# Kernel tuning notes

Hardware: AMD Instinct MI355X
Metric: run time of the kernel (lower is better)

The kernel has to match this reference:

```python
import jax, jax.numpy as jnp
import numpy as np

N_NODES = 100000
N_EDGES = 3200000
IN_DIM = 20
HIDDEN = 64
BN_EPS = 1e-5


def _glorot(key, shape):
    fan_in, fan_out = shape[0], shape[1]
    lim = float(np.sqrt(6.0 / (fan_in + fan_out)))
    return jax.random.uniform(key, shape, jnp.float32, -lim, lim)


def setup_inputs() -> dict:
    key = jax.random.key(0)
    ks = jax.random.split(key, 16)
    xs = jax.random.normal(ks[0], (N_NODES, 6), jnp.float32)
    xt = jax.random.normal(ks[1], (N_NODES, 14), jnp.float32)
    edge_index = jax.random.randint(ks[2], (2, N_EDGES), 0, N_NODES, jnp.int64)
    return {
        "xs": xs,
        "xt": xt,
        "edge_index": edge_index,
        # SAGEConv1: lin_l (neighbors, with bias) + lin_r (root, no bias)
        "W1l": _glorot(ks[3], (IN_DIM, HIDDEN)),
        "b1l": jnp.zeros((HIDDEN,), jnp.float32),
        "W1r": _glorot(ks[4], (IN_DIM, HIDDEN)),
        "g1": jnp.ones((HIDDEN,), jnp.float32),
        "be1": jnp.zeros((HIDDEN,), jnp.float32),
        # SAGEConv2: hidden -> hidden//2
        "W2l": _glorot(ks[5], (HIDDEN, HIDDEN // 2)),
        "b2l": jnp.zeros((HIDDEN // 2,), jnp.float32),
        "W2r": _glorot(ks[6], (HIDDEN, HIDDEN // 2)),
        "g2": jnp.ones((HIDDEN // 2,), jnp.float32),
        "be2": jnp.zeros((HIDDEN // 2,), jnp.float32),
        # embed_proj: Linear(1, 32) + ReLU
        "Wp": _glorot(ks[7], (1, 32)),
        "bp": jnp.zeros((32,), jnp.float32),
        # outage_head: Linear(32, 1)
        "Wo": _glorot(ks[8], (32, 1)),
        "bo": jnp.zeros((1,), jnp.float32),
    }


def _sage_conv(x, src, dst, Wl, bl, Wr):
    # PyG SAGEConv (aggr='mean'): out = lin_l(mean_{j in N(i)} x_j) + lin_r(x_i)
    n = x.shape[0]
    agg = jax.ops.segment_sum(x[src], dst, num_segments=n)           # [N, F] gather+scatter
    deg = jax.ops.segment_sum(jnp.ones_like(dst, x.dtype), dst, num_segments=n)
    mean = agg / jnp.maximum(deg, 1.0)[:, None]
    return mean @ Wl + bl + x @ Wr


def _batchnorm(h, gamma, beta):
    # training-mode BN: biased batch stats over nodes
    m = h.mean(0)
    v = jnp.var(h, axis=0)
    return (h - m) * jax.lax.rsqrt(v + BN_EPS) * gamma + beta


def reference(xs, xt, edge_index, W1l, b1l, W1r, g1, be1,
              W2l, b2l, W2r, g2, be2, Wp, bp, Wo, bo):
    src, dst = edge_index[0], edge_index[1]
    x = jnp.concatenate([xs, xt], axis=-1)                  # [N, 20]
    h = jax.nn.relu(_batchnorm(_sage_conv(x, src, dst, W1l, b1l, W1r), g1, be1))
    h = jax.nn.relu(_batchnorm(_sage_conv(h, src, dst, W2l, b2l, W2r), g2, be2))
    # heads (dropout is identity in eval)
    logit_raw = h.mean(-1, keepdims=True)                   # [N, 1]
    embed = jax.nn.relu(logit_raw @ Wp + bp)                # [N, 32]
    outage_logit = (embed @ Wo + bo)[:, 0]                  # [N]
    return outage_logit
```

## Files before the change

kernel.cpp:

```cpp
#include <hip/hip_runtime.h>
#include <hip/hip_bf16.h>

#define BN_EPS 1e-5f
#define BK_SHIFT 5
#define BK_NODES 32
#define CAP 1280

typedef unsigned short ushort_t;

__device__ inline ushort_t f2bf(float x) {
  unsigned u = __float_as_uint(x);
  unsigned r = (u + 0x7FFFu + ((u >> 16) & 1u)) >> 16;
  return (ushort_t)r;
}
__device__ inline void bf2x(unsigned u, float& a, float& b) {
  a = __uint_as_float(u << 16);
  b = __uint_as_float(u & 0xFFFF0000u);
}

__device__ inline void unpack20(float* ag, uint4 A, uint4 B, uint4 C) {
  float u, v;
  bf2x(A.x, u, v); atomicAdd(ag + 0, u);  atomicAdd(ag + 1, v);
  bf2x(A.y, u, v); atomicAdd(ag + 2, u);  atomicAdd(ag + 3, v);
  bf2x(A.z, u, v); atomicAdd(ag + 4, u);  atomicAdd(ag + 5, v);
  bf2x(A.w, u, v); atomicAdd(ag + 6, u);  atomicAdd(ag + 7, v);
  bf2x(B.x, u, v); atomicAdd(ag + 8, u);  atomicAdd(ag + 9, v);
  bf2x(B.y, u, v); atomicAdd(ag + 10, u); atomicAdd(ag + 11, v);
  bf2x(B.z, u, v); atomicAdd(ag + 12, u); atomicAdd(ag + 13, v);
  bf2x(B.w, u, v); atomicAdd(ag + 14, u); atomicAdd(ag + 15, v);
  bf2x(C.x, u, v); atomicAdd(ag + 16, u); atomicAdd(ag + 17, v);
  bf2x(C.y, u, v); atomicAdd(ag + 18, u); atomicAdd(ag + 19, v);
}

__device__ inline void unpack32(float* ag, uint4 A, uint4 B, uint4 C, uint4 D) {
  float u, v;
  bf2x(A.x, u, v); atomicAdd(ag + 0, u);  atomicAdd(ag + 1, v);
  bf2x(A.y, u, v); atomicAdd(ag + 2, u);  atomicAdd(ag + 3, v);
  bf2x(A.z, u, v); atomicAdd(ag + 4, u);  atomicAdd(ag + 5, v);
  bf2x(A.w, u, v); atomicAdd(ag + 6, u);  atomicAdd(ag + 7, v);
  bf2x(B.x, u, v); atomicAdd(ag + 8, u);  atomicAdd(ag + 9, v);
  bf2x(B.y, u, v); atomicAdd(ag + 10, u); atomicAdd(ag + 11, v);
  bf2x(B.z, u, v); atomicAdd(ag + 12, u); atomicAdd(ag + 13, v);
  bf2x(B.w, u, v); atomicAdd(ag + 14, u); atomicAdd(ag + 15, v);
  bf2x(C.x, u, v); atomicAdd(ag + 16, u); atomicAdd(ag + 17, v);
  bf2x(C.y, u, v); atomicAdd(ag + 18, u); atomicAdd(ag + 19, v);
  bf2x(C.z, u, v); atomicAdd(ag + 20, u); atomicAdd(ag + 21, v);
  bf2x(C.w, u, v); atomicAdd(ag + 22, u); atomicAdd(ag + 23, v);
  bf2x(D.x, u, v); atomicAdd(ag + 24, u); atomicAdd(ag + 25, v);
  bf2x(D.y, u, v); atomicAdd(ag + 26, u); atomicAdd(ag + 27, v);
  bf2x(D.z, u, v); atomicAdd(ag + 28, u); atomicAdd(ag + 29, v);
  bf2x(D.w, u, v); atomicAdd(ag + 30, u); atomicAdd(ag + 31, v);
}

__global__ __launch_bounds__(256) void k_xcat(
    const float* __restrict__ xs, const float* __restrict__ xt,
    ushort_t* __restrict__ xcatp, int N) {
  long i = (long)blockIdx.x * 256 + threadIdx.x;
  if (i >= (long)N * 24) return;
  int n = (int)(i / 24), f = (int)(i - (long)n * 24);
  float v = 0.f;
  if (f < 6) v = xs[(long)n * 6 + f];
  else if (f < 20) v = xt[(long)n * 14 + f - 6];
  xcatp[i] = f2bf(v);
}

__global__ __launch_bounds__(256) void k_scatter_b(
    const int* __restrict__ srcA, const int* __restrict__ dstA,
    unsigned* __restrict__ cursor, unsigned* __restrict__ bucketBuf, int E) {
  long e0 = ((long)blockIdx.x * 256 + threadIdx.x) * 4;
  if (e0 >= E) return;
  if (e0 + 4 <= E) {
    int4 s4 = *(const int4*)(srcA + e0);
    int4 d4 = *(const int4*)(dstA + e0);
    unsigned p0 = atomicAdd(&cursor[(d4.x >> BK_SHIFT) * 16], 1u);
    unsigned p1 = atomicAdd(&cursor[(d4.y >> BK_SHIFT) * 16], 1u);
    unsigned p2 = atomicAdd(&cursor[(d4.z >> BK_SHIFT) * 16], 1u);
    unsigned p3 = atomicAdd(&cursor[(d4.w >> BK_SHIFT) * 16], 1u);
    if (p0 < CAP) bucketBuf[(size_t)(d4.x >> BK_SHIFT) * CAP + p0] =
        ((unsigned)(d4.x & (BK_NODES - 1)) << 17) | (unsigned)s4.x;
    if (p1 < CAP) bucketBuf[(size_t)(d4.y >> BK_SHIFT) * CAP + p1] =
        ((unsigned)(d4.y & (BK_NODES - 1)) << 17) | (unsigned)s4.y;
    if (p2 < CAP) bucketBuf[(size_t)(d4.z >> BK_SHIFT) * CAP + p2] =
        ((unsigned)(d4.z & (BK_NODES - 1)) << 17) | (unsigned)s4.z;
    if (p3 < CAP) bucketBuf[(size_t)(d4.w >> BK_SHIFT) * CAP + p3] =
        ((unsigned)(d4.w & (BK_NODES - 1)) << 17) | (unsigned)s4.w;
  } else {
    for (long e = e0; e < E; ++e) {
      int s = srcA[e], d = dstA[e];
      unsigned pos = atomicAdd(&cursor[(d >> BK_SHIFT) * 16], 1u);
      if (pos < CAP) bucketBuf[(size_t)(d >> BK_SHIFT) * CAP + pos] =
          ((unsigned)(d & (BK_NODES - 1)) << 17) | (unsigned)s;
    }
  }
}

__global__ __launch_bounds__(256, 4) void k_g1(
    const unsigned* __restrict__ cursor, const unsigned* __restrict__ bucketBuf,
    const ushort_t* __restrict__ xcatp,
    const float* __restrict__ xs, const float* __restrict__ xt,
    const float* __restrict__ W1l, const float* __restrict__ b1l,
    const float* __restrict__ W1r,
    float* __restrict__ h1, float* __restrict__ deg_g,
    float* __restrict__ sum1, float* __restrict__ sq1, int N) {
  __shared__ float sWl[1280], sWr[1280];
  __shared__ float aggL[BK_NODES * 21];
  __shared__ float sx[BK_NODES * 20];
  __shared__ float rdeg[BK_NODES];
  __shared__ unsigned degL[BK_NODES];
  __shared__ float ls[256], lq[256];
  int tid = threadIdx.x;
  int b = blockIdx.x;
  int base = b << BK_SHIFT;

  for (int i = tid; i < BK_NODES * 21; i += 256) aggL[i] = 0.f;
  if (tid < BK_NODES) degL[tid] = 0u;
  for (int i = tid; i < 1280; i += 256) { sWl[i] = W1l[i]; sWr[i] = W1r[i]; }
  for (int i = tid; i < BK_NODES * 20; i += 256) {
    int nl = i / 20, f = i - nl * 20;
    int n = base + nl;
    float v = 0.f;
    if (n < N) v = (f < 6) ? xs[(long)n * 6 + f] : xt[(long)n * 14 + f - 6];
    sx[i] = v;
  }
  __syncthreads();

  unsigned cnt = cursor[b * 16];
  if (cnt > CAP) cnt = CAP;
  const unsigned* bb = bucketBuf + (size_t)b * CAP;

  for (unsigned ib = 0; ib < cnt; ib += 1024) {
    unsigned i = ib + ((unsigned)tid << 2);
    if (i >= cnt) continue;
    if (i + 4 <= cnt) {
      uint4 pk4 = *(const uint4*)(bb + i);
      unsigned s0 = pk4.x & 0x1FFFFu, d0 = pk4.x >> 17;
      unsigned s1 = pk4.y & 0x1FFFFu, d1 = pk4.y >> 17;
      unsigned s2 = pk4.z & 0x1FFFFu, d2 = pk4.z >> 17;
      unsigned s3 = pk4.w & 0x1FFFFu, d3 = pk4.w >> 17;
      const uint4* x0 = (const uint4*)(xcatp + (size_t)s0 * 24);
      const uint4* x1 = (const uint4*)(xcatp + (size_t)s1 * 24);
      const uint4* x2 = (const uint4*)(xcatp + (size_t)s2 * 24);
      const uint4* x3 = (const uint4*)(xcatp + (size_t)s3 * 24);
      uint4 a00 = x0[0], a01 = x0[1], a02 = x0[2];
      uint4 a10 = x1[0], a11 = x1[1], a12 = x1[2];
      uint4 a20 = x2[0], a21 = x2[1], a22 = x2[2];
      uint4 a30 = x3[0], a31 = x3[1], a32 = x3[2];
      atomicAdd(&degL[d0], 1u); atomicAdd(&degL[d1], 1u);
      atomicAdd(&degL[d2], 1u); atomicAdd(&degL[d3], 1u);
      unpack20(&aggL[d0 * 21], a00, a01, a02);
      unpack20(&aggL[d1 * 21], a10, a11, a12);
      unpack20(&aggL[d2 * 21], a20, a21, a22);
      unpack20(&aggL[d3 * 21], a30, a31, a32);
    } else {
      for (unsigned j = i; j < cnt; ++j) {
        unsigned pk = bb[j];
        unsigned s = pk & 0x1FFFFu, dl = pk >> 17;
        const uint4* xr = (const uint4*)(xcatp + (size_t)s * 24);
        uint4 A = xr[0], B = xr[1], C = xr[2];
        atomicAdd(&degL[dl], 1u);
        unpack20(&aggL[dl * 21], A, B, C);
      }
    }
  }
  __syncthreads();

  if (tid < BK_NODES) {
    unsigned d = degL[tid];
    rdeg[tid] = 1.f / fmaxf((float)d, 1.f);
    int n = base + tid;
    if (n < N) deg_g[n] = (float)d;
  }
  __syncthreads();
  for (int i = tid; i < BK_NODES * 20; i += 256) {
    int nl = i / 20, f = i - nl * 20;
    aggL[nl * 21 + f] *= rdeg[nl];
  }
  __syncthreads();

  int c = tid & 63;
  float s_acc = 0.f, q_acc = 0.f;
  for (int p = 0; p < 8; ++p) {
    int nl = (tid >> 6) + p * 4;
    int n = base + nl;
    if (n < N) {
      float acc = b1l[c];
#pragma unroll
      for (int f = 0; f < 20; ++f)
        acc += aggL[nl * 21 + f] * sWl[f * 64 + c] + sx[nl * 20 + f] * sWr[f * 64 + c];
      h1[(long)n * 64 + c] = acc;
      s_acc += acc; q_acc += acc * acc;
    }
  }
  ls[tid] = s_acc; lq[tid] = q_acc;
  __syncthreads();
  if (tid < 64) {
    float s = ls[tid], q = lq[tid];
#pragma unroll
    for (int r = 1; r < 4; ++r) { s += ls[tid + 64 * r]; q += lq[tid + 64 * r]; }
    atomicAdd(&sum1[tid], s);
    atomicAdd(&sq1[tid], q);
  }
}

__global__ __launch_bounds__(256) void k_bn1_proj(
    float* __restrict__ h1,
    const float* __restrict__ sum, const float* __restrict__ sq,
    const float* __restrict__ g, const float* __restrict__ be,
    const float* __restrict__ W2l, const float* __restrict__ W2r,
    ushort_t* __restrict__ p2l, int N) {
  __shared__ float sWl[64 * 32], sWr[64 * 32];
  __shared__ float sh[8][64];
  __shared__ float sscale[64], sshift[64];
  int tid = threadIdx.x;
  for (int i = tid; i < 2048; i += 256) { sWl[i] = W2l[i]; sWr[i] = W2r[i]; }
  if (tid < 64) {
    float m = sum[tid] / (float)N;
    float v = sq[tid] / (float)N - m * m;
    float inv = rsqrtf(v + BN_EPS);
    float sc = g[tid] * inv;
    sscale[tid] = sc;
    sshift[tid] = be[tid] - m * sc;
  }
  __syncthreads();
  long base = (long)blockIdx.x * 512;
#pragma unroll
  for (int k = 0; k < 2; ++k) {
    long j = base + tid + k * 256;
    if (j < (long)N * 64) {
      int c = (int)(j & 63);
      float v = h1[j] * sscale[c] + sshift[c];
      sh[(tid + k * 256) >> 6][c] = fmaxf(v, 0.f);
    }
  }
  __syncthreads();
  int c2 = tid & 31, ln = tid >> 5;
  int n = blockIdx.x * 8 + ln;
  if (n < N) {
    float al = 0.f, ar = 0.f;
#pragma unroll
    for (int c = 0; c < 64; ++c) {
      float hv = sh[ln][c];
      al += hv * sWl[c * 32 + c2];
      ar += hv * sWr[c * 32 + c2];
    }
    p2l[(long)n * 32 + c2] = f2bf(al);
    h1[(long)n * 64 + c2] = ar;
  }
}

__global__ __launch_bounds__(256, 4) void k_g2(
    const unsigned* __restrict__ cursor, const unsigned* __restrict__ bucketBuf,
    const ushort_t* __restrict__ p2l, const float* __restrict__ b2l,
    const float* __restrict__ deg_g,
    float* __restrict__ h1,
    float* __restrict__ sum2, float* __restrict__ sq2, int N) {
  __shared__ float aggL[BK_NODES * 33];
  __shared__ float ls[256], lq[256];
  int tid = threadIdx.x;
  int b = blockIdx.x;
  int base = b << BK_SHIFT;
  for (int i = tid; i < BK_NODES * 33; i += 256) aggL[i] = 0.f;
  __syncthreads();
  unsigned cnt = cursor[b * 16];
  if (cnt > CAP) cnt = CAP;
  const unsigned* bb = bucketBuf + (size_t)b * CAP;

  for (unsigned ib = 0; ib < cnt; ib += 1024) {
    unsigned i = ib + ((unsigned)tid << 2);
    if (i >= cnt) continue;
    if (i + 4 <= cnt) {
      uint4 pk4 = *(const uint4*)(bb + i);
      unsigned s0 = pk4.x & 0x1FFFFu, d0 = pk4.x >> 17;
      unsigned s1 = pk4.y & 0x1FFFFu, d1 = pk4.y >> 17;
      unsigned s2 = pk4.z & 0x1FFFFu, d2 = pk4.z >> 17;
      unsigned s3 = pk4.w & 0x1FFFFu, d3 = pk4.w >> 17;
      const uint4* r0 = (const uint4*)(p2l + (size_t)s0 * 32);
      const uint4* r1 = (const uint4*)(p2l + (size_t)s1 * 32);
      const uint4* r2 = (const uint4*)(p2l + (size_t)s2 * 32);
      const uint4* r3 = (const uint4*)(p2l + (size_t)s3 * 32);
      uint4 a00 = r0[0], a01 = r0[1], a02 = r0[2], a03 = r0[3];
      uint4 a10 = r1[0], a11 = r1[1], a12 = r1[2], a13 = r1[3];
      uint4 a20 = r2[0], a21 = r2[1], a22 = r2[2], a23 = r2[3];
      uint4 a30 = r3[0], a31 = r3[1], a32 = r3[2], a33 = r3[3];
      unpack32(&aggL[d0 * 33], a00, a01, a02, a03);
      unpack32(&aggL[d1 * 33], a10, a11, a12, a13);
      unpack32(&aggL[d2 * 33], a20, a21, a22, a23);
      unpack32(&aggL[d3 * 33], a30, a31, a32, a33);
    } else {
      for (unsigned j = i; j < cnt; ++j) {
        unsigned pk = bb[j];
        unsigned s = pk & 0x1FFFFu, dl = pk >> 17;
        const uint4* pr = (const uint4*)(p2l + (size_t)s * 32);
        uint4 A = pr[0], B = pr[1], C = pr[2], D = pr[3];
        unpack32(&aggL[dl * 33], A, B, C, D);
      }
    }
  }
  __syncthreads();

  int c = tid & 31;
  float bc = b2l[c];
  float s_acc = 0.f, q_acc = 0.f;
  for (int p = 0; p < 4; ++p) {
    int nl = (tid >> 5) + p * 8;
    int n = base + nl;
    if (n < N) {
      float rd = 1.f / fmaxf(deg_g[n], 1.f);
      long idx = (long)n * 64 + c;
      float h2 = aggL[nl * 33 + c] * rd + bc + h1[idx];
      h1[idx] = h2;
      s_acc += h2; q_acc += h2 * h2;
    }
  }
  ls[tid] = s_acc; lq[tid] = q_acc;
  __syncthreads();
  if (tid < 32) {
    float s = ls[tid], q = lq[tid];
#pragma unroll
    for (int r = 1; r < 8; ++r) { s += ls[tid + 32 * r]; q += lq[tid + 32 * r]; }
    atomicAdd(&sum2[tid], s);
    atomicAdd(&sq2[tid], q);
  }
}

__global__ __launch_bounds__(256) void k_final(
    const float* __restrict__ h2,
    const float* __restrict__ sum, const float* __restrict__ sq,
    const float* __restrict__ g, const float* __restrict__ be,
    const float* __restrict__ Wp, const float* __restrict__ bp,
    const float* __restrict__ Wo, const float* __restrict__ bo,
    float* __restrict__ out, int N) {
  int tid = threadIdx.x;
  int c = tid & 31, ln = tid >> 5;
  int n = blockIdx.x * 8 + ln;
  if (n >= N) return;
  float m = sum[c] / (float)N;
  float v = sq[c] / (float)N - m * m;
  float inv = rsqrtf(v + BN_EPS);
  float sc = g[c] * inv;
  float sh = be[c] - m * sc;
  float x = fmaxf(h2[(long)n * 64 + c] * sc + sh, 0.f);
#pragma unroll
  for (int msk = 16; msk >= 1; msk >>= 1) x += __shfl_xor(x, msk);
  float lr = x * (1.0f / 32.0f);
  float e = fmaxf(lr * Wp[c] + bp[c], 0.f) * Wo[c];
#pragma unroll
  for (int msk = 16; msk >= 1; msk >>= 1) e += __shfl_xor(e, msk);
  if (c == 0) out[n] = e + bo[0];
}

__global__ __launch_bounds__(256) void k_edge_agg20(
    const int* __restrict__ srcA, const int* __restrict__ dstA,
    const float* __restrict__ xs, const float* __restrict__ xt,
    float* __restrict__ agg, float* __restrict__ deg, int E) {
  long gtid = (long)blockIdx.x * blockDim.x + threadIdx.x;
  int f = (int)(gtid & 31);
  long e = gtid >> 5;
  if (e >= E) return;
  int s = srcA[e], d = dstA[e];
  if (f < 20) {
    float v = (f < 6) ? xs[(long)s * 6 + f] : xt[(long)s * 14 + (f - 6)];
    atomicAdd(&agg[(long)d * 20 + f], v);
  }
  if (f == 0) atomicAdd(&deg[d], 1.0f);
}

__global__ __launch_bounds__(256) void k_sage1(
    const float* __restrict__ agg, const float* __restrict__ deg,
    const float* __restrict__ xs, const float* __restrict__ xt,
    const float* __restrict__ W1l, const float* __restrict__ b1l,
    const float* __restrict__ W1r, float* __restrict__ h1, int N) {
  __shared__ float sWl[1280], sWr[1280];
  __shared__ float sm[4][20], sx[4][20];
  int tid = threadIdx.x;
  for (int i = tid; i < 1280; i += 256) { sWl[i] = W1l[i]; sWr[i] = W1r[i]; }
  int ln = tid >> 6, c = tid & 63;
  int n = blockIdx.x * 4 + ln;
  if (n < N && c < 20) {
    float dv = fmaxf(deg[n], 1.0f);
    sm[ln][c] = agg[(long)n * 20 + c] / dv;
    sx[ln][c] = (c < 6) ? xs[(long)n * 6 + c] : xt[(long)n * 14 + (c - 6)];
  }
  __syncthreads();
  if (n < N) {
    float acc = b1l[c];
#pragma unroll
    for (int f = 0; f < 20; ++f)
      acc += sm[ln][f] * sWl[f * 64 + c] + sx[ln][f] * sWr[f * 64 + c];
    h1[(long)n * 64 + c] = acc;
  }
}

__global__ __launch_bounds__(256) void k_stats(
    const float* __restrict__ h, int N, int C,
    float* __restrict__ sum, float* __restrict__ sq) {
  int tid = threadIdx.x;
  int rows = 256 / C;
  int c = tid % C, r = tid / C;
  float s = 0.f, q = 0.f;
  for (long n = (long)blockIdx.x * rows + r; n < N; n += (long)gridDim.x * rows) {
    float v = h[n * C + c];
    s += v; q += v * v;
  }
  __shared__ float ls[256], lq[256];
  ls[tid] = s; lq[tid] = q;
  __syncthreads();
  if (r == 0) {
    for (int rr = 1; rr < rows; ++rr) { s += ls[c + rr * C]; q += lq[c + rr * C]; }
    atomicAdd(&sum[c], s);
    atomicAdd(&sq[c], q);
  }
}

__global__ __launch_bounds__(256) void k_bn1_proj_fb(
    const float* __restrict__ h1,
    const float* __restrict__ sum, const float* __restrict__ sq,
    const float* __restrict__ g, const float* __restrict__ be,
    const float* __restrict__ W2l, const float* __restrict__ W2r,
    float* __restrict__ p2l, float* __restrict__ p2r, int N) {
  __shared__ float sWl[64 * 32], sWr[64 * 32];
  __shared__ float sh[8][64];
  __shared__ float sscale[64], sshift[64];
  int tid = threadIdx.x;
  for (int i = tid; i < 2048; i += 256) { sWl[i] = W2l[i]; sWr[i] = W2r[i]; }
  if (tid < 64) {
    float m = sum[tid] / (float)N;
    float v = sq[tid] / (float)N - m * m;
    float inv = rsqrtf(v + BN_EPS);
    float sc = g[tid] * inv;
    sscale[tid] = sc;
    sshift[tid] = be[tid] - m * sc;
  }
  __syncthreads();
  long base = (long)blockIdx.x * 512;
#pragma unroll
  for (int k = 0; k < 2; ++k) {
    long j = base + tid + k * 256;
    if (j < (long)N * 64) {
      int c = (int)(j & 63);
      float v = h1[j] * sscale[c] + sshift[c];
      sh[(tid + k * 256) >> 6][c] = fmaxf(v, 0.f);
    }
  }
  __syncthreads();
  int c2 = tid & 31, ln = tid >> 5;
  int n = blockIdx.x * 8 + ln;
  if (n < N) {
    float al = 0.f, ar = 0.f;
#pragma unroll
    for (int c = 0; c < 64; ++c) {
      float hv = sh[ln][c];
      al += hv * sWl[c * 32 + c2];
      ar += hv * sWr[c * 32 + c2];
    }
    p2l[(long)n * 32 + c2] = al;
    p2r[(long)n * 32 + c2] = ar;
  }
}

__global__ __launch_bounds__(256) void k_edge_agg32(
    const int* __restrict__ srcA, const int* __restrict__ dstA,
    const float* __restrict__ p, float* __restrict__ agg, int E) {
  long gtid = (long)blockIdx.x * blockDim.x + threadIdx.x;
  int f = (int)(gtid & 31);
  long e = gtid >> 5;
  if (e >= E) return;
  atomicAdd(&agg[(long)dstA[e] * 32 + f], p[(long)srcA[e] * 32 + f]);
}

__global__ __launch_bounds__(256) void k_h2(
    const float* __restrict__ agg, const float* __restrict__ deg,
    const float* __restrict__ b2l, const float* __restrict__ p2r,
    float* __restrict__ h2, int N) {
  long i = (long)blockIdx.x * blockDim.x + threadIdx.x;
  if (i >= (long)N * 32) return;
  int n = (int)(i >> 5), f = (int)(i & 31);
  float dv = fmaxf(deg[n], 1.0f);
  h2[i] = agg[i] / dv + b2l[f] + p2r[i];
}

__global__ __launch_bounds__(256) void k_final_fb(
    const float* __restrict__ h2,
    const float* __restrict__ sum, const float* __restrict__ sq,
    const float* __restrict__ g, const float* __restrict__ be,
    const float* __restrict__ Wp, const float* __restrict__ bp,
    const float* __restrict__ Wo, const float* __restrict__ bo,
    float* __restrict__ out, int N) {
  int tid = threadIdx.x;
  int c = tid & 31, ln = tid >> 5;
  int n = blockIdx.x * 8 + ln;
  if (n >= N) return;
  float m = sum[c] / (float)N;
  float v = sq[c] / (float)N - m * m;
  float inv = rsqrtf(v + BN_EPS);
  float sc = g[c] * inv;
  float sh = be[c] - m * sc;
  float x = fmaxf(h2[(long)n * 32 + c] * sc + sh, 0.f);
#pragma unroll
  for (int msk = 16; msk >= 1; msk >>= 1) x += __shfl_xor(x, msk);
  float lr = x * (1.0f / 32.0f);
  float e = fmaxf(lr * Wp[c] + bp[c], 0.f) * Wo[c];
#pragma unroll
  for (int msk = 16; msk >= 1; msk >>= 1) e += __shfl_xor(e, msk);
  if (c == 0) out[n] = e + bo[0];
}

extern "C" void kernel_launch(void* const* d_in, const int* in_sizes, int n_in,
                              void* d_out, int out_size, void* d_ws, size_t ws_size,
                              hipStream_t stream) {
  const float* xs  = (const float*)d_in[0];
  const float* xt  = (const float*)d_in[1];
  const int*   ei  = (const int*)d_in[2];
  const float* W1l = (const float*)d_in[3];
  const float* b1l = (const float*)d_in[4];
  const float* W1r = (const float*)d_in[5];
  const float* g1  = (const float*)d_in[6];
  const float* be1 = (const float*)d_in[7];
  const float* W2l = (const float*)d_in[8];
  const float* b2l = (const float*)d_in[9];
  const float* W2r = (const float*)d_in[10];
  const float* g2  = (const float*)d_in[11];
  const float* be2 = (const float*)d_in[12];
  const float* Wp  = (const float*)d_in[13];
  const float* bp  = (const float*)d_in[14];
  const float* Wo  = (const float*)d_in[15];
  const float* bo  = (const float*)d_in[16];
  float* out = (float*)d_out;

  int N = in_sizes[0] / 6;
  int E = in_sizes[2] / 2;
  const int* srcA = ei;
  const int* dstA = ei + E;
  const int tb = 256;
  int NB = (N + BK_NODES - 1) >> BK_SHIFT;

  size_t needB = ((size_t)NB * 16 + (size_t)NB * CAP + (size_t)64 * N +
                  (size_t)16 * N + (size_t)12 * N + (size_t)N + 192) * 4;

  if (ws_size >= needB && N <= (1 << 17)) {
    unsigned* cursor    = (unsigned*)d_ws;
    unsigned* bucketBuf = cursor + (size_t)NB * 16;
    float*    h1        = (float*)(bucketBuf + (size_t)NB * CAP);
    ushort_t* p2l       = (ushort_t*)(h1 + (size_t)64 * N);
    ushort_t* xcatp     = p2l + (size_t)32 * N;
    float*    deg_g     = (float*)(xcatp + (size_t)24 * N);
    float*    stats     = deg_g + (size_t)N;
    float* sum1 = stats, * sq1 = stats + 64, * sum2 = stats + 128, * sq2 = stats + 160;

    hipMemsetAsync(cursor, 0, (size_t)NB * 16 * 4, stream);
    hipMemsetAsync(stats, 0, 192 * 4, stream);

    k_xcat<<<(int)(((long)N * 24 + tb - 1) / tb), tb, 0, stream>>>(xs, xt, xcatp, N);
    k_scatter_b<<<(int)(((long)E + 1023) / 1024), tb, 0, stream>>>(
        srcA, dstA, cursor, bucketBuf, E);
    k_g1<<<NB, tb, 0, stream>>>(cursor, bucketBuf, xcatp, xs, xt,
                                W1l, b1l, W1r, h1, deg_g, sum1, sq1, N);
    k_bn1_proj<<<(N + 7) / 8, tb, 0, stream>>>(h1, sum1, sq1, g1, be1, W2l, W2r, p2l, N);
    k_g2<<<NB, tb, 0, stream>>>(cursor, bucketBuf, p2l, b2l, deg_g, h1, sum2, sq2, N);
    k_final<<<(N + 7) / 8, tb, 0, stream>>>(h1, sum2, sq2, g2, be2, Wp, bp, Wo, bo, out, N);
  } else {
    float* ws   = (float*)d_ws;
    float* deg  = ws;
    float* agg1 = deg + N;
    float* h1   = agg1 + (long)20 * N;
    float* agg2 = h1;
    float* h2   = h1 + (long)32 * N;
    float* p2l  = h1 + (long)64 * N;
    float* p2r  = p2l + (long)32 * N;
    float* stats = p2r + (long)32 * N;
    float* sum1 = stats, * sq1 = stats + 64, * sum2 = stats + 128, * sq2 = stats + 160;

    hipMemsetAsync(deg, 0, sizeof(float) * (size_t)(21 * (long)N), stream);
    hipMemsetAsync(stats, 0, sizeof(float) * 192, stream);

    long t1 = (long)E * 32;
    int eblocks = (int)((t1 + tb - 1) / tb);
    k_edge_agg20<<<eblocks, tb, 0, stream>>>(srcA, dstA, xs, xt, agg1, deg, E);
    k_sage1<<<(N + 3) / 4, tb, 0, stream>>>(agg1, deg, xs, xt, W1l, b1l, W1r, h1, N);
    k_stats<<<1024, tb, 0, stream>>>(h1, N, 64, sum1, sq1);
    k_bn1_proj_fb<<<(N + 7) / 8, tb, 0, stream>>>(h1, sum1, sq1, g1, be1, W2l, W2r, p2l, p2r, N);
    hipMemsetAsync(agg2, 0, sizeof(float) * (size_t)(32 * (long)N), stream);
    k_edge_agg32<<<eblocks, tb, 0, stream>>>(srcA, dstA, p2l, agg2, E);
    k_h2<<<(int)(((long)32 * N + tb - 1) / tb), tb, 0, stream>>>(agg2, deg, b2l, p2r, h2, N);
    k_stats<<<1024, tb, 0, stream>>>(h2, N, 32, sum2, sq2);
    k_final_fb<<<(N + 7) / 8, tb, 0, stream>>>(h2, sum2, sq2, g2, be2, Wp, bp, Wo, bo, out, N);
  }
}
```

Before: 1.181 ms.

## Use nontemporal loads/stores, pad xcat rows to 64B, simplify gather loops

Adds nontemporal load and store builtins across almost every kernel: edge index reads, bucket writes, h1 reads and writes, and deg_g. The bf16 concatenated input rows are padded from 48 to 64 bytes so each row is cache-line aligned. The 4-edge-per-thread gather loops in k_g1 and k_g2 become simple one-edge-per-thread strided loops, which makes the bucket reads coalesced. The occupancy hint in __launch_bounds__ is dropped. Nontemporal hints on data that is reused later (h1, bucketBuf, deg_g) may push it out of L2 and cost extra traffic.

```diff
diff --git a/kernel.cpp b/kernel.cpp
--- a/kernel.cpp
+++ b/kernel.cpp
@@ -7,6 +7,14 @@
 #define CAP 1280
 
 typedef unsigned short ushort_t;
+typedef unsigned int u32x4 __attribute__((ext_vector_type(4)));
+typedef int i32x4 __attribute__((ext_vector_type(4)));
+
+__device__ inline unsigned ntl_u32(const unsigned* p) { return __builtin_nontemporal_load(p); }
+__device__ inline float    ntl_f32(const float* p)    { return __builtin_nontemporal_load(p); }
+__device__ inline void     nts_f32(float* p, float v) { __builtin_nontemporal_store(v, p); }
+__device__ inline void     nts_u32(unsigned* p, unsigned v) { __builtin_nontemporal_store(v, p); }
+__device__ inline i32x4    ntl_i4(const int* p)       { return __builtin_nontemporal_load((const i32x4*)p); }
 
 __device__ inline ushort_t f2bf(float x) {
   unsigned u = __float_as_uint(x);
@@ -18,49 +26,15 @@
   b = __uint_as_float(u & 0xFFFF0000u);
 }
 
-__device__ inline void unpack20(float* ag, uint4 A, uint4 B, uint4 C) {
-  float u, v;
-  bf2x(A.x, u, v); atomicAdd(ag + 0, u);  atomicAdd(ag + 1, v);
-  bf2x(A.y, u, v); atomicAdd(ag + 2, u);  atomicAdd(ag + 3, v);
-  bf2x(A.z, u, v); atomicAdd(ag + 4, u);  atomicAdd(ag + 5, v);
-  bf2x(A.w, u, v); atomicAdd(ag + 6, u);  atomicAdd(ag + 7, v);
-  bf2x(B.x, u, v); atomicAdd(ag + 8, u);  atomicAdd(ag + 9, v);
-  bf2x(B.y, u, v); atomicAdd(ag + 10, u); atomicAdd(ag + 11, v);
-  bf2x(B.z, u, v); atomicAdd(ag + 12, u); atomicAdd(ag + 13, v);
-  bf2x(B.w, u, v); atomicAdd(ag + 14, u); atomicAdd(ag + 15, v);
-  bf2x(C.x, u, v); atomicAdd(ag + 16, u); atomicAdd(ag + 17, v);
-  bf2x(C.y, u, v); atomicAdd(ag + 18, u); atomicAdd(ag + 19, v);
-}
-
-__device__ inline void unpack32(float* ag, uint4 A, uint4 B, uint4 C, uint4 D) {
-  float u, v;
-  bf2x(A.x, u, v); atomicAdd(ag + 0, u);  atomicAdd(ag + 1, v);
-  bf2x(A.y, u, v); atomicAdd(ag + 2, u);  atomicAdd(ag + 3, v);
-  bf2x(A.z, u, v); atomicAdd(ag + 4, u);  atomicAdd(ag + 5, v);
-  bf2x(A.w, u, v); atomicAdd(ag + 6, u);  atomicAdd(ag + 7, v);
-  bf2x(B.x, u, v); atomicAdd(ag + 8, u);  atomicAdd(ag + 9, v);
-  bf2x(B.y, u, v); atomicAdd(ag + 10, u); atomicAdd(ag + 11, v);
-  bf2x(B.z, u, v); atomicAdd(ag + 12, u); atomicAdd(ag + 13, v);
-  bf2x(B.w, u, v); atomicAdd(ag + 14, u); atomicAdd(ag + 15, v);
-  bf2x(C.x, u, v); atomicAdd(ag + 16, u); atomicAdd(ag + 17, v);
-  bf2x(C.y, u, v); atomicAdd(ag + 18, u); atomicAdd(ag + 19, v);
-  bf2x(C.z, u, v); atomicAdd(ag + 20, u); atomicAdd(ag + 21, v);
-  bf2x(C.w, u, v); atomicAdd(ag + 22, u); atomicAdd(ag + 23, v);
-  bf2x(D.x, u, v); atomicAdd(ag + 24, u); atomicAdd(ag + 25, v);
-  bf2x(D.y, u, v); atomicAdd(ag + 26, u); atomicAdd(ag + 27, v);
-  bf2x(D.z, u, v); atomicAdd(ag + 28, u); atomicAdd(ag + 29, v);
-  bf2x(D.w, u, v); atomicAdd(ag + 30, u); atomicAdd(ag + 31, v);
-}
-
 __global__ __launch_bounds__(256) void k_xcat(
     const float* __restrict__ xs, const float* __restrict__ xt,
     ushort_t* __restrict__ xcatp, int N) {
   long i = (long)blockIdx.x * 256 + threadIdx.x;
-  if (i >= (long)N * 24) return;
-  int n = (int)(i / 24), f = (int)(i - (long)n * 24);
+  if (i >= (long)N * 32) return;
+  int n = (int)(i >> 5), f = (int)(i & 31);
   float v = 0.f;
-  if (f < 6) v = xs[(long)n * 6 + f];
-  else if (f < 20) v = xt[(long)n * 14 + f - 6];
+  if (f < 6) v = ntl_f32(&xs[(long)n * 6 + f]);
+  else if (f < 20) v = ntl_f32(&xt[(long)n * 14 + f - 6]);
   xcatp[i] = f2bf(v);
 }
 
@@ -70,31 +44,31 @@
   long e0 = ((long)blockIdx.x * 256 + threadIdx.x) * 4;
   if (e0 >= E) return;
   if (e0 + 4 <= E) {
-    int4 s4 = *(const int4*)(srcA + e0);
-    int4 d4 = *(const int4*)(dstA + e0);
+    i32x4 s4 = ntl_i4(srcA + e0);
+    i32x4 d4 = ntl_i4(dstA + e0);
     unsigned p0 = atomicAdd(&cursor[(d4.x >> BK_SHIFT) * 16], 1u);
     unsigned p1 = atomicAdd(&cursor[(d4.y >> BK_SHIFT) * 16], 1u);
     unsigned p2 = atomicAdd(&cursor[(d4.z >> BK_SHIFT) * 16], 1u);
     unsigned p3 = atomicAdd(&cursor[(d4.w >> BK_SHIFT) * 16], 1u);
-    if (p0 < CAP) bucketBuf[(size_t)(d4.x >> BK_SHIFT) * CAP + p0] =
-        ((unsigned)(d4.x & (BK_NODES - 1)) << 17) | (unsigned)s4.x;
-    if (p1 < CAP) bucketBuf[(size_t)(d4.y >> BK_SHIFT) * CAP + p1] =
-        ((unsigned)(d4.y & (BK_NODES - 1)) << 17) | (unsigned)s4.y;
-    if (p2 < CAP) bucketBuf[(size_t)(d4.z >> BK_SHIFT) * CAP + p2] =
-        ((unsigned)(d4.z & (BK_NODES - 1)) << 17) | (unsigned)s4.z;
-    if (p3 < CAP) bucketBuf[(size_t)(d4.w >> BK_SHIFT) * CAP + p3] =
-        ((unsigned)(d4.w & (BK_NODES - 1)) << 17) | (unsigned)s4.w;
+    if (p0 < CAP) nts_u32(&bucketBuf[(size_t)(d4.x >> BK_SHIFT) * CAP + p0],
+        ((unsigned)(d4.x & (BK_NODES - 1)) << 17) | (unsigned)s4.x);
+    if (p1 < CAP) nts_u32(&bucketBuf[(size_t)(d4.y >> BK_SHIFT) * CAP + p1],
+        ((unsigned)(d4.y & (BK_NODES - 1)) << 17) | (unsigned)s4.y);
+    if (p2 < CAP) nts_u32(&bucketBuf[(size_t)(d4.z >> BK_SHIFT) * CAP + p2],
+        ((unsigned)(d4.z & (BK_NODES - 1)) << 17) | (unsigned)s4.z);
+    if (p3 < CAP) nts_u32(&bucketBuf[(size_t)(d4.w >> BK_SHIFT) * CAP + p3],
+        ((unsigned)(d4.w & (BK_NODES - 1)) << 17) | (unsigned)s4.w);
   } else {
     for (long e = e0; e < E; ++e) {
       int s = srcA[e], d = dstA[e];
       unsigned pos = atomicAdd(&cursor[(d >> BK_SHIFT) * 16], 1u);
-      if (pos < CAP) bucketBuf[(size_t)(d >> BK_SHIFT) * CAP + pos] =
-          ((unsigned)(d & (BK_NODES - 1)) << 17) | (unsigned)s;
-    }
-  }
-}
-
-__global__ __launch_bounds__(256, 4) void k_g1(
+      if (pos < CAP) nts_u32(&bucketBuf[(size_t)(d >> BK_SHIFT) * CAP + pos],
+          ((unsigned)(d & (BK_NODES - 1)) << 17) | (unsigned)s);
+    }
+  }
+}
+
+__global__ __launch_bounds__(256) void k_g1(
     const unsigned* __restrict__ cursor, const unsigned* __restrict__ bucketBuf,
     const ushort_t* __restrict__ xcatp,
     const float* __restrict__ xs, const float* __restrict__ xt,
@@ -119,7 +93,7 @@
     int nl = i / 20, f = i - nl * 20;
     int n = base + nl;
     float v = 0.f;
-    if (n < N) v = (f < 6) ? xs[(long)n * 6 + f] : xt[(long)n * 14 + f - 6];
+    if (n < N) v = (f < 6) ? ntl_f32(&xs[(long)n * 6 + f]) : ntl_f32(&xt[(long)n * 14 + f - 6]);
     sx[i] = v;
   }
   __syncthreads();
@@ -128,39 +102,25 @@
   if (cnt > CAP) cnt = CAP;
   const unsigned* bb = bucketBuf + (size_t)b * CAP;
 
-  for (unsigned ib = 0; ib < cnt; ib += 1024) {
-    unsigned i = ib + ((unsigned)tid << 2);
-    if (i >= cnt) continue;
-    if (i + 4 <= cnt) {
-      uint4 pk4 = *(const uint4*)(bb + i);
-      unsigned s0 = pk4.x & 0x1FFFFu, d0 = pk4.x >> 17;
-      unsigned s1 = pk4.y & 0x1FFFFu, d1 = pk4.y >> 17;
-      unsigned s2 = pk4.z & 0x1FFFFu, d2 = pk4.z >> 17;
-      unsigned s3 = pk4.w & 0x1FFFFu, d3 = pk4.w >> 17;
-      const uint4* x0 = (const uint4*)(xcatp + (size_t)s0 * 24);
-      const uint4* x1 = (const uint4*)(xcatp + (size_t)s1 * 24);
-      const uint4* x2 = (const uint4*)(xcatp + (size_t)s2 * 24);
-      const uint4* x3 = (const uint4*)(xcatp + (size_t)s3 * 24);
-      uint4 a00 = x0[0], a01 = x0[1], a02 = x0[2];
-      uint4 a10 = x1[0], a11 = x1[1], a12 = x1[2];
-      uint4 a20 = x2[0], a21 = x2[1], a22 = x2[2];
-      uint4 a30 = x3[0], a31 = x3[1], a32 = x3[2];
-      atomicAdd(&degL[d0], 1u); atomicAdd(&degL[d1], 1u);
-      atomicAdd(&degL[d2], 1u); atomicAdd(&degL[d3], 1u);
-      unpack20(&aggL[d0 * 21], a00, a01, a02);
-      unpack20(&aggL[d1 * 21], a10, a11, a12);
-      unpack20(&aggL[d2 * 21], a20, a21, a22);
-      unpack20(&aggL[d3 * 21], a30, a31, a32);
-    } else {
-      for (unsigned j = i; j < cnt; ++j) {
-        unsigned pk = bb[j];
-        unsigned s = pk & 0x1FFFFu, dl = pk >> 17;
-        const uint4* xr = (const uint4*)(xcatp + (size_t)s * 24);
-        uint4 A = xr[0], B = xr[1], C = xr[2];
-        atomicAdd(&degL[dl], 1u);
-        unpack20(&aggL[dl * 21], A, B, C);
-      }
-    }
+  for (unsigned i = tid; i < cnt; i += 256) {
+    unsigned pk = ntl_u32(bb + i);
+    int s = (int)(pk & 0x1FFFFu);
+    int dl = (int)(pk >> 17);
+    const u32x4* xr = (const u32x4*)(xcatp + (size_t)s * 32);
+    u32x4 A = xr[0], B = xr[1], C = xr[2];
+    atomicAdd(&degL[dl], 1u);
+    float* ag = &aggL[dl * 21];
+    float u, v;
+    bf2x(A.x, u, v); atomicAdd(ag + 0, u);  atomicAdd(ag + 1, v);
+    bf2x(A.y, u, v); atomicAdd(ag + 2, u);  atomicAdd(ag + 3, v);
+    bf2x(A.z, u, v); atomicAdd(ag + 4, u);  atomicAdd(ag + 5, v);
+    bf2x(A.w, u, v); atomicAdd(ag + 6, u);  atomicAdd(ag + 7, v);
+    bf2x(B.x, u, v); atomicAdd(ag + 8, u);  atomicAdd(ag + 9, v);
+    bf2x(B.y, u, v); atomicAdd(ag + 10, u); atomicAdd(ag + 11, v);
+    bf2x(B.z, u, v); atomicAdd(ag + 12, u); atomicAdd(ag + 13, v);
+    bf2x(B.w, u, v); atomicAdd(ag + 14, u); atomicAdd(ag + 15, v);
+    bf2x(C.x, u, v); atomicAdd(ag + 16, u); atomicAdd(ag + 17, v);
+    bf2x(C.y, u, v); atomicAdd(ag + 18, u); atomicAdd(ag + 19, v);
   }
   __syncthreads();
 
@@ -168,7 +128,7 @@
     unsigned d = degL[tid];
     rdeg[tid] = 1.f / fmaxf((float)d, 1.f);
     int n = base + tid;
-    if (n < N) deg_g[n] = (float)d;
+    if (n < N) nts_f32(&deg_g[n], (float)d);
   }
   __syncthreads();
   for (int i = tid; i < BK_NODES * 20; i += 256) {
@@ -187,7 +147,7 @@
 #pragma unroll
       for (int f = 0; f < 20; ++f)
         acc += aggL[nl * 21 + f] * sWl[f * 64 + c] + sx[nl * 20 + f] * sWr[f * 64 + c];
-      h1[(long)n * 64 + c] = acc;
+      nts_f32(&h1[(long)n * 64 + c], acc);
       s_acc += acc; q_acc += acc * acc;
     }
   }
@@ -228,7 +188,7 @@
     long j = base + tid + k * 256;
     if (j < (long)N * 64) {
       int c = (int)(j & 63);
-      float v = h1[j] * sscale[c] + sshift[c];
+      float v = ntl_f32(&h1[j]) * sscale[c] + sshift[c];
       sh[(tid + k * 256) >> 6][c] = fmaxf(v, 0.f);
     }
   }
@@ -244,11 +204,11 @@
       ar += hv * sWr[c * 32 + c2];
     }
     p2l[(long)n * 32 + c2] = f2bf(al);
-    h1[(long)n * 64 + c2] = ar;
-  }
-}
-
-__global__ __launch_bounds__(256, 4) void k_g2(
+    nts_f32(&h1[(long)n * 64 + c2], ar);
+  }
+}
+
+__global__ __launch_bounds__(256) void k_g2(
     const unsigned* __restrict__ cursor, const unsigned* __restrict__ bucketBuf,
     const ushort_t* __restrict__ p2l, const float* __restrict__ b2l,
     const float* __restrict__ deg_g,
@@ -265,36 +225,30 @@
   if (cnt > CAP) cnt = CAP;
   const unsigned* bb = bucketBuf + (size_t)b * CAP;
 
-  for (unsigned ib = 0; ib < cnt; ib += 1024) {
-    unsigned i = ib + ((unsigned)tid << 2);
-    if (i >= cnt) continue;
-    if (i + 4 <= cnt) {
-      uint4 pk4 = *(const uint4*)(bb + i);
-      unsigned s0 = pk4.x & 0x1FFFFu, d0 = pk4.x >> 17;
-      unsigned s1 = pk4.y & 0x1FFFFu, d1 = pk4.y >> 17;
-      unsigned s2 = pk4.z & 0x1FFFFu, d2 = pk4.z >> 17;
-      unsigned s3 = pk4.w & 0x1FFFFu, d3 = pk4.w >> 17;
-      const uint4* r0 = (const uint4*)(p2l + (size_t)s0 * 32);
-      const uint4* r1 = (const uint4*)(p2l + (size_t)s1 * 32);
-      const uint4* r2 = (const uint4*)(p2l + (size_t)s2 * 32);
-      const uint4* r3 = (const uint4*)(p2l + (size_t)s3 * 32);
-      uint4 a00 = r0[0], a01 = r0[1], a02 = r0[2], a03 = r0[3];
-      uint4 a10 = r1[0], a11 = r1[1], a12 = r1[2], a13 = r1[3];
-      uint4 a20 = r2[0], a21 = r2[1], a22 = r2[2], a23 = r2[3];
-      uint4 a30 = r3[0], a31 = r3[1], a32 = r3[2], a33 = r3[3];
-      unpack32(&aggL[d0 * 33], a00, a01, a02, a03);
-      unpack32(&aggL[d1 * 33], a10, a11, a12, a13);
-      unpack32(&aggL[d2 * 33], a20, a21, a22, a23);
-      unpack32(&aggL[d3 * 33], a30, a31, a32, a33);
-    } else {
-      for (unsigned j = i; j < cnt; ++j) {
-        unsigned pk = bb[j];
-        unsigned s = pk & 0x1FFFFu, dl = pk >> 17;
-        const uint4* pr = (const uint4*)(p2l + (size_t)s * 32);
-        uint4 A = pr[0], B = pr[1], C = pr[2], D = pr[3];
-        unpack32(&aggL[dl * 33], A, B, C, D);
-      }
-    }
+  for (unsigned i = tid; i < cnt; i += 256) {
+    unsigned pk = ntl_u32(bb + i);
+    int s = (int)(pk & 0x1FFFFu);
+    int dl = (int)(pk >> 17);
+    const u32x4* pr = (const u32x4*)(p2l + (size_t)s * 32);
+    u32x4 A = pr[0], B = pr[1], C = pr[2], D = pr[3];
+    float* ag = &aggL[dl * 33];
+    float u, v;
+    bf2x(A.x, u, v); atomicAdd(ag + 0, u);  atomicAdd(ag + 1, v);
+    bf2x(A.y, u, v); atomicAdd(ag + 2, u);  atomicAdd(ag + 3, v);
+    bf2x(A.z, u, v); atomicAdd(ag + 4, u);  atomicAdd(ag + 5, v);
+    bf2x(A.w, u, v); atomicAdd(ag + 6, u);  atomicAdd(ag + 7, v);
+    bf2x(B.x, u, v); atomicAdd(ag + 8, u);  atomicAdd(ag + 9, v);
+    bf2x(B.y, u, v); atomicAdd(ag + 10, u); atomicAdd(ag + 11, v);
+    bf2x(B.z, u, v); atomicAdd(ag + 12, u); atomicAdd(ag + 13, v);
+    bf2x(B.w, u, v); atomicAdd(ag + 14, u); atomicAdd(ag + 15, v);
+    bf2x(C.x, u, v); atomicAdd(ag + 16, u); atomicAdd(ag + 17, v);
+    bf2x(C.y, u, v); atomicAdd(ag + 18, u); atomicAdd(ag + 19, v);
+    bf2x(C.z, u, v); atomicAdd(ag + 20, u); atomicAdd(ag + 21, v);
+    bf2x(C.w, u, v); atomicAdd(ag + 22, u); atomicAdd(ag + 23, v);
+    bf2x(D.x, u, v); atomicAdd(ag + 24, u); atomicAdd(ag + 25, v);
+    bf2x(D.y, u, v); atomicAdd(ag + 26, u); atomicAdd(ag + 27, v);
+    bf2x(D.z, u, v); atomicAdd(ag + 28, u); atomicAdd(ag + 29, v);
+    bf2x(D.w, u, v); atomicAdd(ag + 30, u); atomicAdd(ag + 31, v);
   }
   __syncthreads();
 
@@ -305,10 +259,10 @@
     int nl = (tid >> 5) + p * 8;
     int n = base + nl;
     if (n < N) {
-      float rd = 1.f / fmaxf(deg_g[n], 1.f);
+      float rd = 1.f / fmaxf(ntl_f32(&deg_g[n]), 1.f);
       long idx = (long)n * 64 + c;
-      float h2 = aggL[nl * 33 + c] * rd + bc + h1[idx];
-      h1[idx] = h2;
+      float h2 = aggL[nl * 33 + c] * rd + bc + ntl_f32(&h1[idx]);
+      nts_f32(&h1[idx], h2);
       s_acc += h2; q_acc += h2 * h2;
     }
   }
@@ -339,7 +293,7 @@
   float inv = rsqrtf(v + BN_EPS);
   float sc = g[c] * inv;
   float sh = be[c] - m * sc;
-  float x = fmaxf(h2[(long)n * 64 + c] * sc + sh, 0.f);
+  float x = fmaxf(ntl_f32(&h2[(long)n * 64 + c]) * sc + sh, 0.f);
 #pragma unroll
   for (int msk = 16; msk >= 1; msk >>= 1) x += __shfl_xor(x, msk);
   float lr = x * (1.0f / 32.0f);
@@ -535,7 +489,7 @@
   int NB = (N + BK_NODES - 1) >> BK_SHIFT;
 
   size_t needB = ((size_t)NB * 16 + (size_t)NB * CAP + (size_t)64 * N +
-                  (size_t)16 * N + (size_t)12 * N + (size_t)N + 192) * 4;
+                  (size_t)16 * N + (size_t)16 * N + (size_t)N + 192) * 4;
 
   if (ws_size >= needB && N <= (1 << 17)) {
     unsigned* cursor    = (unsigned*)d_ws;
@@ -543,14 +497,14 @@
     float*    h1        = (float*)(bucketBuf + (size_t)NB * CAP);
     ushort_t* p2l       = (ushort_t*)(h1 + (size_t)64 * N);
     ushort_t* xcatp     = p2l + (size_t)32 * N;
-    float*    deg_g     = (float*)(xcatp + (size_t)24 * N);
+    float*    deg_g     = (float*)(xcatp + (size_t)32 * N);
     float*    stats     = deg_g + (size_t)N;
     float* sum1 = stats, * sq1 = stats + 64, * sum2 = stats + 128, * sq2 = stats + 160;
 
     hipMemsetAsync(cursor, 0, (size_t)NB * 16 * 4, stream);
     hipMemsetAsync(stats, 0, 192 * 4, stream);
 
-    k_xcat<<<(int)(((long)N * 24 + tb - 1) / tb), tb, 0, stream>>>(xs, xt, xcatp, N);
+    k_xcat<<<(int)(((long)N * 32 + tb - 1) / tb), tb, 0, stream>>>(xs, xt, xcatp, N);
     k_scatter_b<<<(int)(((long)E + 1023) / 1024), tb, 0, stream>>>(
         srcA, dstA, cursor, bucketBuf, E);
     k_g1<<<NB, tb, 0, stream>>>(cursor, bucketBuf, xcatp, xs, xt,
```

Result: slower. 1.250 ms (+5.8%).
